# Performance work log

Measured on AMD Instinct MI355X. Metric: run time of the kernel, lower is better.

Reference implementation:

```python
import jax, jax.numpy as jnp
import numpy as np


def setup_inputs() -> dict:
    key = jax.random.key(0)
    k1, k2, k3, k4, k5 = jax.random.split(key, 5)
    B, heads, H, W = 64, 16, 256, 256
    bottleneck = heads // 4  # SE_Parameter = 4
    relation = jax.random.normal(k1, (B, heads, H, W), dtype=jnp.float32)
    # torch.nn.Linear weights: [out_features, in_features]
    W1 = jax.random.normal(k2, (bottleneck, heads), dtype=jnp.float32) * (1.0 / np.sqrt(heads))
    b1 = jax.random.normal(k3, (bottleneck,), dtype=jnp.float32) * 0.01
    W2 = jax.random.normal(k4, (heads, bottleneck), dtype=jnp.float32) * (1.0 / np.sqrt(bottleneck))
    b2 = jax.random.normal(k5, (heads,), dtype=jnp.float32) * 0.01
    return {"relation": relation, "W1": W1, "b1": b1, "W2": W2, "b2": b2}


def reference(relation, W1, b1, W2, b2):
    # GAP over spatial dims: [B, heads]
    gap = jnp.mean(relation, axis=(2, 3))
    # two-layer SE bottleneck with relu + sigmoid gate
    bottle = jax.nn.relu(jnp.einsum("bh,ch->bc", gap, W1) + b1)
    gate = jax.nn.sigmoid(jnp.einsum("bc,hc->bh", bottle, W2) + b2)
    # Original code does output[0,0,i,j].long(): truncate-to-int cast of the gate
    # (faithful to the source, even though sigmoid in (0,1) truncates to 0).
    scale = gate.astype(jnp.int64).astype(relation.dtype)  # [B, heads]
    # fused broadcast multiply replaces the Python double loop
    return relation * scale[:, :, None, None]
```

## Files before the change

### kernel.cpp

```cpp
#include <hip/hip_runtime.h>


#define NB 64
#define NHEADS 16
#define NPLANES (NB * NHEADS)
#define HW 65536
#define HW4 16384
#define GAP_THREADS 512
#define MUL_CHUNKS 8
#define CHUNK4 (HW4 / MUL_CHUNKS)

typedef float f32x4 __attribute__((ext_vector_type(4)));

__global__ __launch_bounds__(GAP_THREADS) void se_gap_kernel(const float* __restrict__ rel,
                                                             float* __restrict__ gap) {
    const int p = blockIdx.x;
    const f32x4* __restrict__ src = (const f32x4*)(rel + (size_t)p * HW);
    float s = 0.0f;
    #pragma unroll 4
    for (int i = threadIdx.x; i < HW4; i += GAP_THREADS) {
        f32x4 v = __builtin_nontemporal_load(src + i);
        s += (v.x + v.y) + (v.z + v.w);
    }
    #pragma unroll
    for (int off = 32; off > 0; off >>= 1)
        s += __shfl_down(s, off, 64);
    __shared__ float ws[GAP_THREADS / 64];
    const int wave = threadIdx.x >> 6;
    if ((threadIdx.x & 63) == 0) ws[wave] = s;
    __syncthreads();
    if (threadIdx.x == 0) {
        float t = 0.0f;
        #pragma unroll
        for (int w = 0; w < GAP_THREADS / 64; ++w) t += ws[w];
        gap[p] = t * (1.0f / (float)HW);
    }
}

__global__ __launch_bounds__(256) void se_mlp_mul_kernel(const float* __restrict__ rel,
                                                         const float* __restrict__ gap,
                                                         const float* __restrict__ W1,
                                                         const float* __restrict__ b1,
                                                         const float* __restrict__ W2,
                                                         const float* __restrict__ b2,
                                                         float* __restrict__ out) {
    const int p     = blockIdx.x >> 3;
    const int chunk = blockIdx.x & (MUL_CHUNKS - 1);
    const int b = p >> 4;
    const int h = p & (NHEADS - 1);

    float bot[4];
    #pragma unroll
    for (int c = 0; c < 4; ++c) {
        float acc = b1[c];
        #pragma unroll
        for (int k = 0; k < NHEADS; ++k) acc += gap[b * NHEADS + k] * W1[c * NHEADS + k];
        bot[c] = fmaxf(acc, 0.0f);
    }
    float acc = b2[h];
    #pragma unroll
    for (int c = 0; c < 4; ++c) acc += bot[c] * W2[h * 4 + c];
    const float gate = 1.0f / (1.0f + expf(-acc));
    const float s = (float)(long long)gate;

    const size_t base4 = (size_t)p * HW4 + (size_t)chunk * CHUNK4;
    f32x4* __restrict__ dst = (f32x4*)out + base4;
    if (s == 0.0f) {
        const f32x4 z = {0.0f, 0.0f, 0.0f, 0.0f};
        for (int i = threadIdx.x; i < CHUNK4; i += 256)
            __builtin_nontemporal_store(z, dst + i);
    } else {
        const f32x4* __restrict__ src = (const f32x4*)rel + base4;
        for (int i = threadIdx.x; i < CHUNK4; i += 256) {
            f32x4 v = __builtin_nontemporal_load(src + i);
            v *= s;
            __builtin_nontemporal_store(v, dst + i);
        }
    }
}

extern "C" void kernel_launch(void* const* d_in, const int* in_sizes, int n_in,
                              void* d_out, int out_size, void* d_ws, size_t ws_size,
                              hipStream_t stream) {
    const float* rel = (const float*)d_in[0];
    const float* W1  = (const float*)d_in[1];
    const float* b1  = (const float*)d_in[2];
    const float* W2  = (const float*)d_in[3];
    const float* b2  = (const float*)d_in[4];
    float* out = (float*)d_out;

    float* gap = (float*)d_ws;

    se_gap_kernel<<<NPLANES, GAP_THREADS, 0, stream>>>(rel, gap);
    se_mlp_mul_kernel<<<NPLANES * MUL_CHUNKS, 256, 0, stream>>>(rel, gap, W1, b1, W2, b2, out);
}
```

Before: 93.94 us.

## Fuse GAP, SE MLP and scaling into one kernel with per-batch atomic barrier

Replaces the separate GAP and MLP-multiply kernels with one fused kernel. Each block reduces half a plane, atomically adds its partial sum, then spins on a per-batch counter until all 32 producer blocks of that batch arrive. It then computes the SE gate and writes the scaled (usually zero) output. This removes a kernel boundary and the tail/launch gap between phases. It adds a small init kernel and an inter-block spin barrier that relies on all blocks of a batch being co-resident, which risks deadlock or stalls if scheduling does not guarantee that.

Result: slower. 291.9 us (+210.7%).

```diff
diff --git a/kernel.cpp b/kernel.cpp
--- a/kernel.cpp
+++ b/kernel.cpp
@@ -6,74 +6,90 @@
 #define NPLANES (NB * NHEADS)
 #define HW 65536
 #define HW4 16384
-#define GAP_THREADS 512
-#define MUL_CHUNKS 8
-#define CHUNK4 (HW4 / MUL_CHUNKS)
+#define BLOCKS_PER_PLANE 2
+#define CHUNK4 (HW4 / BLOCKS_PER_PLANE)
+#define NBLOCKS (NPLANES * BLOCKS_PER_PLANE)
+#define PRODUCERS_PER_BATCH (NHEADS * BLOCKS_PER_PLANE)
 
 typedef float f32x4 __attribute__((ext_vector_type(4)));
 
-__global__ __launch_bounds__(GAP_THREADS) void se_gap_kernel(const float* __restrict__ rel,
-                                                             float* __restrict__ gap) {
-    const int p = blockIdx.x;
-    const f32x4* __restrict__ src = (const f32x4*)(rel + (size_t)p * HW);
+__global__ __launch_bounds__(256) void se_init_kernel(float* __restrict__ acc,
+                                                      int* __restrict__ cnt) {
+    const int i = threadIdx.x + blockIdx.x * 256;
+    if (i < NPLANES) acc[i] = 0.0f;
+    if (i < NB) cnt[i] = 0;
+}
+
+__global__ __launch_bounds__(256, 8) void se_fused_kernel(const float* __restrict__ rel,
+                                                          const float* __restrict__ W1,
+                                                          const float* __restrict__ b1,
+                                                          const float* __restrict__ W2,
+                                                          const float* __restrict__ b2,
+                                                          float* __restrict__ out,
+                                                          float* __restrict__ acc,
+                                                          int* __restrict__ cnt) {
+    const int blk = blockIdx.x;
+    const int p = blk >> 1;
+    const int q = blk & 1;
+    const int b = p >> 4;
+    const int h = p & (NHEADS - 1);
+
+    const size_t base4 = (size_t)p * HW4 + (size_t)q * CHUNK4;
+    const f32x4* __restrict__ src = (const f32x4*)rel + base4;
     float s = 0.0f;
-    #pragma unroll 4
-    for (int i = threadIdx.x; i < HW4; i += GAP_THREADS) {
+    #pragma unroll 8
+    for (int i = threadIdx.x; i < CHUNK4; i += 256) {
         f32x4 v = __builtin_nontemporal_load(src + i);
         s += (v.x + v.y) + (v.z + v.w);
     }
     #pragma unroll
     for (int off = 32; off > 0; off >>= 1)
         s += __shfl_down(s, off, 64);
-    __shared__ float ws[GAP_THREADS / 64];
-    const int wave = threadIdx.x >> 6;
-    if ((threadIdx.x & 63) == 0) ws[wave] = s;
+    __shared__ float sm[4];
+    if ((threadIdx.x & 63) == 0) sm[threadIdx.x >> 6] = s;
     __syncthreads();
+
+    __shared__ float scale_sm;
     if (threadIdx.x == 0) {
-        float t = 0.0f;
+        const float t = (sm[0] + sm[1]) + (sm[2] + sm[3]);
+        __hip_atomic_fetch_add(acc + p, t, __ATOMIC_RELAXED, __HIP_MEMORY_SCOPE_AGENT);
+        __hip_atomic_fetch_add(cnt + b, 1, __ATOMIC_RELEASE, __HIP_MEMORY_SCOPE_AGENT);
+        while (__hip_atomic_load(cnt + b, __ATOMIC_ACQUIRE, __HIP_MEMORY_SCOPE_AGENT)
+               < PRODUCERS_PER_BATCH)
+            __builtin_amdgcn_s_sleep(2);
+        float g[NHEADS];
         #pragma unroll
-        for (int w = 0; w < GAP_THREADS / 64; ++w) t += ws[w];
-        gap[p] = t * (1.0f / (float)HW);
+        for (int k = 0; k < NHEADS; ++k)
+            g[k] = __hip_atomic_load(acc + (b * NHEADS + k), __ATOMIC_RELAXED,
+                                     __HIP_MEMORY_SCOPE_AGENT) * (1.0f / (float)HW);
+        float bot[4];
+        #pragma unroll
+        for (int c = 0; c < 4; ++c) {
+            float a = b1[c];
+            #pragma unroll
+            for (int k = 0; k < NHEADS; ++k) a += g[k] * W1[c * NHEADS + k];
+            bot[c] = fmaxf(a, 0.0f);
+        }
+        float a = b2[h];
+        #pragma unroll
+        for (int c = 0; c < 4; ++c) a += bot[c] * W2[h * 4 + c];
+        const float gate = 1.0f / (1.0f + expf(-a));
+        scale_sm = (float)(long long)gate;
     }
-}
+    __syncthreads();
+    const float sc = scale_sm;
 
-__global__ __launch_bounds__(256) void se_mlp_mul_kernel(const float* __restrict__ rel,
-                                                         const float* __restrict__ gap,
-                                                         const float* __restrict__ W1,
-                                                         const float* __restrict__ b1,
-                                                         const float* __restrict__ W2,
-                                                         const float* __restrict__ b2,
-                                                         float* __restrict__ out) {
-    const int p     = blockIdx.x >> 3;
-    const int chunk = blockIdx.x & (MUL_CHUNKS - 1);
-    const int b = p >> 4;
-    const int h = p & (NHEADS - 1);
-
-    float bot[4];
-    #pragma unroll
-    for (int c = 0; c < 4; ++c) {
-        float acc = b1[c];
-        #pragma unroll
-        for (int k = 0; k < NHEADS; ++k) acc += gap[b * NHEADS + k] * W1[c * NHEADS + k];
-        bot[c] = fmaxf(acc, 0.0f);
-    }
-    float acc = b2[h];
-    #pragma unroll
-    for (int c = 0; c < 4; ++c) acc += bot[c] * W2[h * 4 + c];
-    const float gate = 1.0f / (1.0f + expf(-acc));
-    const float s = (float)(long long)gate;
-
-    const size_t base4 = (size_t)p * HW4 + (size_t)chunk * CHUNK4;
     f32x4* __restrict__ dst = (f32x4*)out + base4;
-    if (s == 0.0f) {
+    if (sc == 0.0f) {
         const f32x4 z = {0.0f, 0.0f, 0.0f, 0.0f};
+        #pragma unroll 8
         for (int i = threadIdx.x; i < CHUNK4; i += 256)
             __builtin_nontemporal_store(z, dst + i);
     } else {
-        const f32x4* __restrict__ src = (const f32x4*)rel + base4;
+        #pragma unroll 4
         for (int i = threadIdx.x; i < CHUNK4; i += 256) {
             f32x4 v = __builtin_nontemporal_load(src + i);
-            v *= s;
+            v *= sc;
             __builtin_nontemporal_store(v, dst + i);
         }
     }
@@ -89,8 +105,9 @@
     const float* b2  = (const float*)d_in[4];
     float* out = (float*)d_out;
 
-    float* gap = (float*)d_ws;
+    float* acc = (float*)d_ws;
+    int*   cnt = (int*)((float*)d_ws + NPLANES);
 
-    se_gap_kernel<<<NPLANES, GAP_THREADS, 0, stream>>>(rel, gap);
-    se_mlp_mul_kernel<<<NPLANES * MUL_CHUNKS, 256, 0, stream>>>(rel, gap, W1, b1, W2, b2, out);
+    se_init_kernel<<<4, 256, 0, stream>>>(acc, cnt);
+    se_fused_kernel<<<NBLOCKS, 256, 0, stream>>>(rel, W1, b1, W2, b2, out, acc, cnt);
 }
```

## Pre-zero output in separate kernel and only rescale planes with nonzero gate

Applied to the files above, without the earlier changes.

Adds a standalone zero-fill kernel over the whole output that does not depend on the gate. The old fused MLP+multiply kernel becomes a per-plane fixup that returns early when the truncated gate is zero and otherwise overwrites the plane with the scaled input. The aim is to make the zero-write a simple streaming store that no longer waits on the GAP result. In exchange it adds a third kernel launch, and any plane with a nonzero gate is written twice. All three kernels run on the same stream, so the zero-fill still runs in sequence with the GAP read rather than overlapping it.

Result: slower. 97.39 us (+3.7%).

```diff
diff --git a/kernel.cpp b/kernel.cpp
--- a/kernel.cpp
+++ b/kernel.cpp
@@ -7,10 +7,18 @@
 #define HW 65536
 #define HW4 16384
 #define GAP_THREADS 512
-#define MUL_CHUNKS 8
-#define CHUNK4 (HW4 / MUL_CHUNKS)
+#define FILL_BLOCKS 2048
+#define FILL_CHUNK4 (HW4 * NPLANES / FILL_BLOCKS)
 
 typedef float f32x4 __attribute__((ext_vector_type(4)));
+
+__global__ __launch_bounds__(256) void se_zero_kernel(float* __restrict__ out) {
+    f32x4* __restrict__ dst = (f32x4*)out + (size_t)blockIdx.x * FILL_CHUNK4;
+    const f32x4 z = {0.0f, 0.0f, 0.0f, 0.0f};
+    #pragma unroll 8
+    for (int i = threadIdx.x; i < FILL_CHUNK4; i += 256)
+        __builtin_nontemporal_store(z, dst + i);
+}
 
 __global__ __launch_bounds__(GAP_THREADS) void se_gap_kernel(const float* __restrict__ rel,
                                                              float* __restrict__ gap) {
@@ -37,45 +45,40 @@
     }
 }
 
-__global__ __launch_bounds__(256) void se_mlp_mul_kernel(const float* __restrict__ rel,
-                                                         const float* __restrict__ gap,
-                                                         const float* __restrict__ W1,
-                                                         const float* __restrict__ b1,
-                                                         const float* __restrict__ W2,
-                                                         const float* __restrict__ b2,
-                                                         float* __restrict__ out) {
-    const int p     = blockIdx.x >> 3;
-    const int chunk = blockIdx.x & (MUL_CHUNKS - 1);
+__global__ __launch_bounds__(256) void se_fixup_kernel(const float* __restrict__ rel,
+                                                       const float* __restrict__ gap,
+                                                       const float* __restrict__ W1,
+                                                       const float* __restrict__ b1,
+                                                       const float* __restrict__ W2,
+                                                       const float* __restrict__ b2,
+                                                       float* __restrict__ out) {
+    const int p = blockIdx.x;
     const int b = p >> 4;
     const int h = p & (NHEADS - 1);
 
     float bot[4];
     #pragma unroll
     for (int c = 0; c < 4; ++c) {
-        float acc = b1[c];
+        float a = b1[c];
         #pragma unroll
-        for (int k = 0; k < NHEADS; ++k) acc += gap[b * NHEADS + k] * W1[c * NHEADS + k];
-        bot[c] = fmaxf(acc, 0.0f);
+        for (int k = 0; k < NHEADS; ++k) a += gap[b * NHEADS + k] * W1[c * NHEADS + k];
+        bot[c] = fmaxf(a, 0.0f);
     }
-    float acc = b2[h];
+    float a = b2[h];
     #pragma unroll
-    for (int c = 0; c < 4; ++c) acc += bot[c] * W2[h * 4 + c];
-    const float gate = 1.0f / (1.0f + expf(-acc));
-    const float s = (float)(long long)gate;
+    for (int c = 0; c < 4; ++c) a += bot[c] * W2[h * 4 + c];
+    const float gate = 1.0f / (1.0f + expf(-a));
+    const float sc = (float)(long long)gate;
+    if (sc == 0.0f) return;
 
-    const size_t base4 = (size_t)p * HW4 + (size_t)chunk * CHUNK4;
+    const size_t base4 = (size_t)p * HW4;
+    const f32x4* __restrict__ src = (const f32x4*)rel + base4;
     f32x4* __restrict__ dst = (f32x4*)out + base4;
-    if (s == 0.0f) {
-        const f32x4 z = {0.0f, 0.0f, 0.0f, 0.0f};
-        for (int i = threadIdx.x; i < CHUNK4; i += 256)
-            __builtin_nontemporal_store(z, dst + i);
-    } else {
-        const f32x4* __restrict__ src = (const f32x4*)rel + base4;
-        for (int i = threadIdx.x; i < CHUNK4; i += 256) {
-            f32x4 v = __builtin_nontemporal_load(src + i);
-            v *= s;
-            __builtin_nontemporal_store(v, dst + i);
-        }
+    #pragma unroll 4
+    for (int i = threadIdx.x; i < HW4; i += 256) {
+        f32x4 v = __builtin_nontemporal_load(src + i);
+        v *= sc;
+        __builtin_nontemporal_store(v, dst + i);
     }
 }
 
@@ -91,6 +94,7 @@
 
     float* gap = (float*)d_ws;
 
+    se_zero_kernel<<<FILL_BLOCKS, 256, 0, stream>>>(out);
     se_gap_kernel<<<NPLANES, GAP_THREADS, 0, stream>>>(rel, gap);
-    se_mlp_mul_kernel<<<NPLANES * MUL_CHUNKS, 256, 0, stream>>>(rel, gap, W1, b1, W2, b2, out);
+    se_fixup_kernel<<<NPLANES, 256, 0, stream>>>(rel, gap, W1, b1, W2, b2, out);
 }
```
